# Optimization experiments

Measured on AMD Instinct MI355X. Metric: run time of the kernel, lower is better.

Reference implementation:

```python
import jax, jax.numpy as jnp
import numpy as np

B, N, C, O, K, D = 32, 2048, 64, 64, 3, 16

def setup_inputs() -> dict:
    key = jax.random.key(0)
    ks = jax.random.split(key, 6)
    x = jax.random.normal(ks[0], (B, N, C), dtype=jnp.float32)
    node_embeddings = jax.random.normal(ks[1], (N, D), dtype=jnp.float32)
    adj_m = jax.random.uniform(ks[2], (N, N), dtype=jnp.float32)
    weights_pool = jax.random.normal(ks[3], (D, K, C, O), dtype=jnp.float32) * 0.1
    bias_pool = jax.random.normal(ks[4], (D, O), dtype=jnp.float32) * 0.1
    sa_weight = jax.random.normal(ks[5], (N, 2 * N), dtype=jnp.float32) * (1.0 / np.sqrt(2 * N))
    return {"x": x, "node_embeddings": node_embeddings, "adj_m": adj_m,
            "weights_pool": weights_pool, "bias_pool": bias_pool, "sa_weight": sa_weight}

def reference(x, node_embeddings, adj_m, weights_pool, bias_pool, sa_weight):
    n = node_embeddings.shape[0]
    # learned adaptive adjacency [N,N]
    supports = jax.nn.softmax(jax.nn.relu(node_embeddings @ node_embeddings.T), axis=1)
    # SpatialAttention: 1x1 conv over 2N channels == matmul with [N,2N] weight
    z = jnp.concatenate([supports, adj_m], axis=1) @ sa_weight.T  # [N,N]
    s2 = jax.nn.sigmoid(z)
    supports = s2 * adj_m + (1.0 - s2) * supports
    # Chebyshev polynomial basis
    support_set = [jnp.eye(n, dtype=supports.dtype), supports]
    for _ in range(2, K):
        support_set.append(2.0 * supports @ support_set[-1] - support_set[-2])
    supports_k = jnp.stack(support_set, axis=0)  # [K,N,N]
    # per-node generated weights/bias from embeddings
    weights = jnp.einsum('nd,dkio->nkio', node_embeddings, weights_pool)  # [N,K,C,O]
    bias = node_embeddings @ bias_pool  # [N,O]
    # graph conv: aggregate then per-node matmul
    x_g = jnp.einsum('knm,bmc->bnkc', supports_k, x)  # [B,N,K,C]
    x_gconv = jnp.einsum('bnki,nkio->bno', x_g, weights) + bias  # [B,N,O]
    return x_gconv
```

## Files before the change

kernel.cpp:

```cpp
#include <hip/hip_runtime.h>


typedef unsigned short u16;
typedef float f32x4 __attribute__((ext_vector_type(4)));
typedef __bf16 bf16x8 __attribute__((ext_vector_type(8)));
typedef unsigned short u16x8 __attribute__((ext_vector_type(8)));

__device__ __forceinline__ u16 f2bf(float f) {
    unsigned u = __float_as_uint(f);
    u += 0x7FFFu + ((u >> 16) & 1u);
    return (u16)(u >> 16);
}
__device__ __forceinline__ float bf2f(u16 h) {
    return __uint_as_float((unsigned)h << 16);
}
__device__ __forceinline__ void gl_lds16(const void* g, void* l) {
    __builtin_amdgcn_global_load_lds(
        (const __attribute__((address_space(1))) unsigned*)g,
        (__attribute__((address_space(3))) unsigned*)l, 16, 0, 0);
}

__global__ __launch_bounds__(256)
void supports_softmax(const float* __restrict__ E, u16* __restrict__ Acat) {
    const int n = blockIdx.x, tid = threadIdx.x;
    const int lane = tid & 63, wave = tid >> 6;
    __shared__ float red[4];
    float e[16];
#pragma unroll
    for (int d = 0; d < 16; ++d) e[d] = E[n * 16 + d];
    float v[8];
    float mx = 0.f;
#pragma unroll
    for (int r = 0; r < 8; ++r) {
        int m = r * 256 + tid;
        const float4* Er = (const float4*)(E + (size_t)m * 16);
        float4 a = Er[0], b = Er[1], c = Er[2], d4 = Er[3];
        float s = 0.f;
        s = fmaf(a.x, e[0], s);  s = fmaf(a.y, e[1], s);
        s = fmaf(a.z, e[2], s);  s = fmaf(a.w, e[3], s);
        s = fmaf(b.x, e[4], s);  s = fmaf(b.y, e[5], s);
        s = fmaf(b.z, e[6], s);  s = fmaf(b.w, e[7], s);
        s = fmaf(c.x, e[8], s);  s = fmaf(c.y, e[9], s);
        s = fmaf(c.z, e[10], s); s = fmaf(c.w, e[11], s);
        s = fmaf(d4.x, e[12], s); s = fmaf(d4.y, e[13], s);
        s = fmaf(d4.z, e[14], s); s = fmaf(d4.w, e[15], s);
        s = fmaxf(s, 0.f);
        v[r] = s;
        mx = fmaxf(mx, s);
    }
    for (int off = 32; off; off >>= 1) mx = fmaxf(mx, __shfl_down(mx, off, 64));
    if (lane == 0) red[wave] = mx;
    __syncthreads();
    mx = fmaxf(fmaxf(red[0], red[1]), fmaxf(red[2], red[3]));
    __syncthreads();
    float sum = 0.f;
#pragma unroll
    for (int r = 0; r < 8; ++r) { v[r] = __expf(v[r] - mx); sum += v[r]; }
    for (int off = 32; off; off >>= 1) sum += __shfl_down(sum, off, 64);
    if (lane == 0) red[wave] = sum;
    __syncthreads();
    sum = red[0] + red[1] + red[2] + red[3];
    float inv = 1.f / sum;
#pragma unroll
    for (int r = 0; r < 8; ++r)
        Acat[(size_t)n * 4096 + r * 256 + tid] = f2bf(v[r] * inv);
}

__global__ __launch_bounds__(256)
void cast_inputs(const float* __restrict__ adj, const float* __restrict__ saw,
                 u16* __restrict__ Acat, u16* __restrict__ sawb) {
    int bid = blockIdx.x;
    if (bid < 4096) {
        size_t j = ((size_t)bid * 256 + threadIdx.x) * 4;
        float4 v = *(const float4*)(adj + j);
        int n = (int)(j >> 11), c = (int)(j & 2047);
        ushort4 o = make_ushort4(f2bf(v.x), f2bf(v.y), f2bf(v.z), f2bf(v.w));
        *(ushort4*)(Acat + (size_t)n * 4096 + 2048 + c) = o;
    } else {
        size_t j = ((size_t)(bid - 4096) * 256 + threadIdx.x) * 4;
        float4 v = *(const float4*)(saw + j);
        ushort4 o = make_ushort4(f2bf(v.x), f2bf(v.y), f2bf(v.z), f2bf(v.w));
        *(ushort4*)(sawb + j) = o;
    }
}

__global__ __launch_bounds__(256)
void build_xtT(const float* __restrict__ x, u16* __restrict__ xtT) {
    __shared__ u16 t[64][65];
    int b = blockIdx.y, m0 = blockIdx.x * 64;
    int c = threadIdx.x & 63, g = threadIdx.x >> 6;
#pragma unroll
    for (int r = 0; r < 16; ++r) {
        int mm = g * 16 + r;
        t[mm][c] = f2bf(x[((size_t)b * 2048 + m0 + mm) * 64 + c]);
    }
    __syncthreads();
#pragma unroll
    for (int r = 0; r < 16; ++r) {
        int cc = g * 16 + r;
        xtT[((size_t)b * 64 + cc) * 2048 + m0 + c] = t[c][cc];
    }
}

__global__ __launch_bounds__(256, 4)
void gemm_bt(const u16* __restrict__ A, const u16* __restrict__ Bt,
             float* __restrict__ Cf, int M, int N, int K, int Kh) {
    __shared__ alignas(16) u16 As[128 * 64];
    __shared__ alignas(16) u16 Bs[64 * 64];
    const int tid = threadIdx.x, lane = tid & 63, wave = tid >> 6;
    const int m0 = blockIdx.y * 128, n0 = blockIdx.x * 64;
    const int wm = (wave >> 1) * 64, wn = (wave & 1) * 32;
    const int kbeg = blockIdx.z * Kh, kend = kbeg + Kh;
    const int ml = lane & 15, c0l = lane >> 4;
    f32x4 acc[4][2] = {};

    int baseA[4], mskA[4], baseB[2], mskB[2];
#pragma unroll
    for (int i = 0; i < 4; ++i) { int m = wm + i * 16 + ml; baseA[i] = m * 8; mskA[i] = m & 7; }
#pragma unroll
    for (int j = 0; j < 2; ++j) { int nn = wn + j * 16 + ml; baseB[j] = nn * 8; mskB[j] = nn & 7; }

    for (int k0 = kbeg; k0 < kend; k0 += 64) {
#pragma unroll
        for (int r = 0; r < 4; ++r) {
            int s = wave * 64 + r * 256 + lane;
            int row = s >> 3, gc = (s & 7) ^ (row & 7);
            u16* lds = As + (wave * 64 + r * 256) * 8;
            gl_lds16(A + (size_t)(m0 + row) * K + k0 + gc * 8, lds);
        }
#pragma unroll
        for (int r = 0; r < 2; ++r) {
            int s = wave * 64 + r * 256 + lane;
            int row = s >> 3, gc = (s & 7) ^ (row & 7);
            u16* lds = Bs + (wave * 64 + r * 256) * 8;
            gl_lds16(Bt + (size_t)(n0 + row) * K + k0 + gc * 8, lds);
        }
        __syncthreads();
#pragma unroll
        for (int ks8 = 0; ks8 < 8; ks8 += 4) {
            bf16x8 af[4], bv[2];
#pragma unroll
            for (int i = 0; i < 4; ++i)
                af[i] = *(const bf16x8*)(As + (baseA[i] + ((c0l + ks8) ^ mskA[i])) * 8);
#pragma unroll
            for (int j = 0; j < 2; ++j)
                bv[j] = *(const bf16x8*)(Bs + (baseB[j] + ((c0l + ks8) ^ mskB[j])) * 8);
#pragma unroll
            for (int i = 0; i < 4; ++i)
#pragma unroll
                for (int j = 0; j < 2; ++j)
                    acc[i][j] = __builtin_amdgcn_mfma_f32_16x16x32_bf16(af[i], bv[j], acc[i][j], 0, 0, 0);
        }
        __syncthreads();
    }

    const int col_l = lane & 15, row_l = (lane >> 4) * 4;
    float* Cfp = Cf + (size_t)blockIdx.z * M * N;
#pragma unroll
    for (int i = 0; i < 4; ++i)
#pragma unroll
        for (int j = 0; j < 2; ++j)
#pragma unroll
            for (int r = 0; r < 4; ++r) {
                int row = m0 + wm + i * 16 + row_l + r;
                int col = n0 + wn + j * 16 + col_l;
                Cfp[(size_t)row * N + col] = acc[i][j][r];
            }
}

__global__ __launch_bounds__(256)
void reduce_z(const float* __restrict__ p, const float* __restrict__ adj,
              const u16* __restrict__ Acat, u16* __restrict__ S) {
    size_t j = ((size_t)blockIdx.x * 256 + threadIdx.x) * 4;
    float4 a = *(const float4*)(p + j);
    float4 b = *(const float4*)(p + (size_t)2048 * 2048 + j);
    float4 ad = *(const float4*)(adj + j);
    int row = (int)(j >> 11), col = (int)(j & 2047);
    ushort4 sp = *(const ushort4*)(Acat + (size_t)row * 4096 + col);
    float z0 = a.x + b.x, z1 = a.y + b.y, z2 = a.z + b.z, z3 = a.w + b.w;
    float s0 = 1.f / (1.f + __expf(-z0)), s1 = 1.f / (1.f + __expf(-z1));
    float s2 = 1.f / (1.f + __expf(-z2)), s3 = 1.f / (1.f + __expf(-z3));
    ushort4 o = make_ushort4(
        f2bf(s0 * ad.x + (1.f - s0) * bf2f(sp.x)),
        f2bf(s1 * ad.y + (1.f - s1) * bf2f(sp.y)),
        f2bf(s2 * ad.z + (1.f - s2) * bf2f(sp.z)),
        f2bf(s3 * ad.w + (1.f - s3) * bf2f(sp.w)));
    *(ushort4*)(S + j) = o;
}

__global__ __launch_bounds__(256)
void reduceT(const float* __restrict__ p, u16* __restrict__ xg1,
             u16* __restrict__ xg1T) {
    __shared__ u16 t[64][65];
    int bx = blockIdx.x * 64, by = blockIdx.y * 64;
    int c = threadIdx.x & 63, g = threadIdx.x >> 6;
#pragma unroll
    for (int r = 0; r < 16; ++r) {
        int row = g * 16 + r;
        size_t idx = (size_t)(by + row) * 2048 + bx + c;
        u16 v = f2bf(p[idx] + p[(size_t)2048 * 2048 + idx]);
        xg1[idx] = v;
        t[row][c] = v;
    }
    __syncthreads();
#pragma unroll
    for (int r = 0; r < 16; ++r) {
        int row = g * 16 + r;
        xg1T[(size_t)(bx + row) * 2048 + by + c] = t[c][row];
    }
}

__global__ __launch_bounds__(256)
void reduce2(const float* __restrict__ p, u16* __restrict__ xg2) {
    size_t j = ((size_t)blockIdx.x * 256 + threadIdx.x) * 4;
    float4 a = *(const float4*)(p + j);
    float4 b = *(const float4*)(p + (size_t)2048 * 2048 + j);
    *(ushort4*)(xg2 + j) = make_ushort4(f2bf(a.x + b.x), f2bf(a.y + b.y),
                                        f2bf(a.z + b.z), f2bf(a.w + b.w));
}

__global__ __launch_bounds__(256)
void wgen(const float* __restrict__ E, const float* __restrict__ Wp,
          u16* __restrict__ Wn) {
    __shared__ float Es[128 * 16];
    const int tid = threadIdx.x;
    const int c0 = blockIdx.x * 512, nb = blockIdx.y * 128;
    const int i4 = (tid & 127) * 4, ng = tid >> 7;
    for (int j = tid; j < 2048; j += 256) Es[j] = E[nb * 16 + j];
    float4 wpv[16];
#pragma unroll
    for (int d = 0; d < 16; ++d)
        wpv[d] = *(const float4*)(Wp + (size_t)d * 12288 + c0 + i4);
    __syncthreads();
    for (int nl = 0; nl < 64; ++nl) {
        int n = ng * 64 + nl;
        float4 s = make_float4(0.f, 0.f, 0.f, 0.f);
#pragma unroll
        for (int d = 0; d < 16; ++d) {
            float e = Es[n * 16 + d];
            s.x = fmaf(e, wpv[d].x, s.x);
            s.y = fmaf(e, wpv[d].y, s.y);
            s.z = fmaf(e, wpv[d].z, s.z);
            s.w = fmaf(e, wpv[d].w, s.w);
        }
        ushort4 o = make_ushort4(f2bf(s.x), f2bf(s.y), f2bf(s.z), f2bf(s.w));
        *(ushort4*)(Wn + (size_t)(nb + n) * 12288 + c0 + i4) = o;
    }
}

__global__ __launch_bounds__(256, 4)
void gconv(const float* __restrict__ x, const float* __restrict__ E,
           const u16* __restrict__ Wn, const float* __restrict__ bp,
           const u16* __restrict__ xg1, const u16* __restrict__ xg2,
           float* __restrict__ out) {
    const int n = blockIdx.x, tid = threadIdx.x;
    __shared__ alignas(16) u16 wl[3 * 64 * 64];
    __shared__ alignas(16) u16 xl[3 * 32 * 72];
    __shared__ float bl[64];
    const u16* wrow = Wn + (size_t)n * 12288;
    for (int j = tid * 8; j < 12288; j += 2048)
        *(u16x8*)(wl + j) = *(const u16x8*)(wrow + j);
    if (tid < 64) {
        float s = 0.f;
#pragma unroll
        for (int d = 0; d < 16; ++d) s = fmaf(E[n * 16 + d], bp[d * 64 + tid], s);
        bl[tid] = s;
    }
    {
        const int b = tid >> 3, i = (tid & 7) * 8;
        *(u16x8*)(xl + 2304 + b * 72 + i) = *(const u16x8*)(xg1 + (size_t)n * 2048 + tid * 8);
        *(u16x8*)(xl + 4608 + b * 72 + i) = *(const u16x8*)(xg2 + (size_t)n * 2048 + tid * 8);
        float4 xa = *(const float4*)(x + ((size_t)b * 2048 + n) * 64 + i);
        float4 xb = *(const float4*)(x + ((size_t)b * 2048 + n) * 64 + i + 4);
        u16x8 xc;
        xc[0] = f2bf(xa.x); xc[1] = f2bf(xa.y); xc[2] = f2bf(xa.z); xc[3] = f2bf(xa.w);
        xc[4] = f2bf(xb.x); xc[5] = f2bf(xb.y); xc[6] = f2bf(xb.z); xc[7] = f2bf(xb.w);
        *(u16x8*)(xl + b * 72 + i) = xc;
    }
    __syncthreads();
    for (int j = tid * 8; j < 4096; j += 2048) {
        u16x8 w0 = *(const u16x8*)(wl + j);
        u16x8 w2 = *(const u16x8*)(wl + 8192 + j);
        u16x8 o0, o2;
#pragma unroll
        for (int t = 0; t < 8; ++t) {
            float f2 = bf2f(w2[t]);
            o0[t] = f2bf(bf2f(w0[t]) - f2);
            o2[t] = f2bf(2.f * f2);
        }
        *(u16x8*)(wl + j) = o0;
        *(u16x8*)(wl + 8192 + j) = o2;
    }
    __syncthreads();
    const int b = tid >> 3, og = tid & 7;
    float acc[8];
#pragma unroll
    for (int t = 0; t < 8; ++t) acc[t] = bl[og * 8 + t];
#pragma unroll
    for (int k = 0; k < 3; ++k) {
        const u16* xr = xl + k * 2304 + b * 72;
        const u16* wr = wl + k * 4096 + og * 8;
#pragma unroll 4
        for (int i = 0; i < 64; ++i) {
            float xv = bf2f(xr[i]);
            u16x8 w = *(const u16x8*)(wr + i * 64);
            acc[0] = fmaf(bf2f(w[0]), xv, acc[0]);
            acc[1] = fmaf(bf2f(w[1]), xv, acc[1]);
            acc[2] = fmaf(bf2f(w[2]), xv, acc[2]);
            acc[3] = fmaf(bf2f(w[3]), xv, acc[3]);
            acc[4] = fmaf(bf2f(w[4]), xv, acc[4]);
            acc[5] = fmaf(bf2f(w[5]), xv, acc[5]);
            acc[6] = fmaf(bf2f(w[6]), xv, acc[6]);
            acc[7] = fmaf(bf2f(w[7]), xv, acc[7]);
        }
    }
    float* op = out + ((size_t)b * 2048 + n) * 64 + og * 8;
    *(float4*)op       = make_float4(acc[0], acc[1], acc[2], acc[3]);
    *((float4*)op + 1) = make_float4(acc[4], acc[5], acc[6], acc[7]);
}

extern "C" void kernel_launch(void* const* d_in, const int* in_sizes, int n_in,
                              void* d_out, int out_size, void* d_ws, size_t ws_size,
                              hipStream_t stream) {
    const float* x   = (const float*)d_in[0];
    const float* E   = (const float*)d_in[1];
    const float* adj = (const float*)d_in[2];
    const float* Wp  = (const float*)d_in[3];
    const float* bp  = (const float*)d_in[4];
    const float* saw = (const float*)d_in[5];
    float* out = (float*)d_out;

    char* ws = (char*)d_ws;
    const size_t MB = 1u << 20;
    u16*   Acat  = (u16*)(ws);
    u16*   sawb  = (u16*)(ws + 16 * MB);
    u16*   XtT   = (u16*)(ws + 32 * MB);
    float* part  = (float*)(ws + 48 * MB);
    u16*   S_bf  = (u16*)(ws + 16 * MB);
    u16*   xg1T  = (u16*)(ws + 24 * MB);
    u16*   xg1_bf= (u16*)(ws);
    u16*   xg2_bf= (u16*)(ws + 8 * MB);
    u16*   Wn    = (u16*)(ws + 24 * MB);

    supports_softmax<<<2048, 256, 0, stream>>>(E, Acat);
    cast_inputs<<<12288, 256, 0, stream>>>(adj, saw, Acat, sawb);
    build_xtT<<<dim3(32, 32), 256, 0, stream>>>(x, XtT);

    gemm_bt<<<dim3(32, 16, 2), 256, 0, stream>>>(Acat, sawb, part, 2048, 2048, 4096, 2048);
    reduce_z<<<4096, 256, 0, stream>>>(part, adj, Acat, S_bf);
    gemm_bt<<<dim3(32, 16, 2), 256, 0, stream>>>(S_bf, XtT, part, 2048, 2048, 2048, 1024);
    reduceT<<<dim3(32, 32), 256, 0, stream>>>(part, xg1_bf, xg1T);
    gemm_bt<<<dim3(32, 16, 2), 256, 0, stream>>>(S_bf, xg1T, part, 2048, 2048, 2048, 1024);
    reduce2<<<4096, 256, 0, stream>>>(part, xg2_bf);

    wgen<<<dim3(24, 16), 256, 0, stream>>>(E, Wp, Wn);
    gconv<<<2048, 256, 0, stream>>>(x, E, Wn, bp, xg1_bf, xg2_bf, out);
}
```

Before: 331.0 us.

## Reassociate per-node gconv through weights pool on MFMA; widen split-K GEMM tiles

Stops materializing the per-node generated weights [N,K,C,O]. The graph convolution becomes sum_d E[n,d]*(X_cat @ Wpool_d), computed with MFMA, with the Chebyshev identity/T2 terms folded into the pool weights. The main GEMM moves to 128x128 tiles with 4-way split-K and bf16 partials, halving partial traffic at the cost of extra bf16 rounding in the reductions. x is cast to bf16 up front, and layouts are changed so xg1/xg2 are stored batch-major for the new gconv.

Result: faster. 306.2 us (-7.5%).

```diff
diff --git a/kernel.cpp b/kernel.cpp
--- a/kernel.cpp
+++ b/kernel.cpp
@@ -68,7 +68,8 @@
 
 __global__ __launch_bounds__(256)
 void cast_inputs(const float* __restrict__ adj, const float* __restrict__ saw,
-                 u16* __restrict__ Acat, u16* __restrict__ sawb) {
+                 const float* __restrict__ x, u16* __restrict__ Acat,
+                 u16* __restrict__ sawb, u16* __restrict__ x_bf) {
     int bid = blockIdx.x;
     if (bid < 4096) {
         size_t j = ((size_t)bid * 256 + threadIdx.x) * 4;
@@ -76,11 +77,16 @@
         int n = (int)(j >> 11), c = (int)(j & 2047);
         ushort4 o = make_ushort4(f2bf(v.x), f2bf(v.y), f2bf(v.z), f2bf(v.w));
         *(ushort4*)(Acat + (size_t)n * 4096 + 2048 + c) = o;
-    } else {
+    } else if (bid < 12288) {
         size_t j = ((size_t)(bid - 4096) * 256 + threadIdx.x) * 4;
         float4 v = *(const float4*)(saw + j);
         ushort4 o = make_ushort4(f2bf(v.x), f2bf(v.y), f2bf(v.z), f2bf(v.w));
         *(ushort4*)(sawb + j) = o;
+    } else {
+        size_t j = ((size_t)(bid - 12288) * 256 + threadIdx.x) * 4;
+        float4 v = *(const float4*)(x + j);
+        ushort4 o = make_ushort4(f2bf(v.x), f2bf(v.y), f2bf(v.z), f2bf(v.w));
+        *(ushort4*)(x_bf + j) = o;
     }
 }
 
@@ -102,82 +108,86 @@
     }
 }
 
-__global__ __launch_bounds__(256, 4)
+__global__ __launch_bounds__(256, 3)
 void gemm_bt(const u16* __restrict__ A, const u16* __restrict__ Bt,
-             float* __restrict__ Cf, int M, int N, int K, int Kh) {
+             u16* __restrict__ Cp, int M, int N, int K, int Kh) {
     __shared__ alignas(16) u16 As[128 * 64];
-    __shared__ alignas(16) u16 Bs[64 * 64];
+    __shared__ alignas(16) u16 Bs[128 * 64];
     const int tid = threadIdx.x, lane = tid & 63, wave = tid >> 6;
-    const int m0 = blockIdx.y * 128, n0 = blockIdx.x * 64;
-    const int wm = (wave >> 1) * 64, wn = (wave & 1) * 32;
+    const int m0 = blockIdx.y * 128, n0 = blockIdx.x * 128;
+    const int wm = (wave >> 1) * 64, wn = (wave & 1) * 64;
     const int kbeg = blockIdx.z * Kh, kend = kbeg + Kh;
     const int ml = lane & 15, c0l = lane >> 4;
-    f32x4 acc[4][2] = {};
-
-    int baseA[4], mskA[4], baseB[2], mskB[2];
+    f32x4 acc[4][4] = {};
+
+    int baseA[4], mskA[4], baseB[4], mskB[4];
 #pragma unroll
     for (int i = 0; i < 4; ++i) { int m = wm + i * 16 + ml; baseA[i] = m * 8; mskA[i] = m & 7; }
 #pragma unroll
-    for (int j = 0; j < 2; ++j) { int nn = wn + j * 16 + ml; baseB[j] = nn * 8; mskB[j] = nn & 7; }
+    for (int j = 0; j < 4; ++j) { int nn = wn + j * 16 + ml; baseB[j] = nn * 8; mskB[j] = nn & 7; }
 
     for (int k0 = kbeg; k0 < kend; k0 += 64) {
 #pragma unroll
         for (int r = 0; r < 4; ++r) {
             int s = wave * 64 + r * 256 + lane;
             int row = s >> 3, gc = (s & 7) ^ (row & 7);
-            u16* lds = As + (wave * 64 + r * 256) * 8;
-            gl_lds16(A + (size_t)(m0 + row) * K + k0 + gc * 8, lds);
-        }
-#pragma unroll
-        for (int r = 0; r < 2; ++r) {
+            gl_lds16(A + (size_t)(m0 + row) * K + k0 + gc * 8, As + (size_t)s * 8);
+        }
+#pragma unroll
+        for (int r = 0; r < 4; ++r) {
             int s = wave * 64 + r * 256 + lane;
             int row = s >> 3, gc = (s & 7) ^ (row & 7);
-            u16* lds = Bs + (wave * 64 + r * 256) * 8;
-            gl_lds16(Bt + (size_t)(n0 + row) * K + k0 + gc * 8, lds);
+            gl_lds16(Bt + (size_t)(n0 + row) * K + k0 + gc * 8, Bs + (size_t)s * 8);
         }
         __syncthreads();
 #pragma unroll
-        for (int ks8 = 0; ks8 < 8; ks8 += 4) {
-            bf16x8 af[4], bv[2];
+        for (int ks4 = 0; ks4 < 8; ks4 += 4) {
+            bf16x8 af[4], bv[4];
 #pragma unroll
             for (int i = 0; i < 4; ++i)
-                af[i] = *(const bf16x8*)(As + (baseA[i] + ((c0l + ks8) ^ mskA[i])) * 8);
-#pragma unroll
-            for (int j = 0; j < 2; ++j)
-                bv[j] = *(const bf16x8*)(Bs + (baseB[j] + ((c0l + ks8) ^ mskB[j])) * 8);
+                af[i] = *(const bf16x8*)(As + (baseA[i] + ((c0l + ks4) ^ mskA[i])) * 8);
+#pragma unroll
+            for (int j = 0; j < 4; ++j)
+                bv[j] = *(const bf16x8*)(Bs + (baseB[j] + ((c0l + ks4) ^ mskB[j])) * 8);
 #pragma unroll
             for (int i = 0; i < 4; ++i)
 #pragma unroll
-                for (int j = 0; j < 2; ++j)
+                for (int j = 0; j < 4; ++j)
                     acc[i][j] = __builtin_amdgcn_mfma_f32_16x16x32_bf16(af[i], bv[j], acc[i][j], 0, 0, 0);
         }
         __syncthreads();
     }
 
     const int col_l = lane & 15, row_l = (lane >> 4) * 4;
-    float* Cfp = Cf + (size_t)blockIdx.z * M * N;
+    u16* Cz = Cp + (size_t)blockIdx.z * M * N;
 #pragma unroll
     for (int i = 0; i < 4; ++i)
 #pragma unroll
-        for (int j = 0; j < 2; ++j)
+        for (int j = 0; j < 4; ++j)
 #pragma unroll
             for (int r = 0; r < 4; ++r) {
                 int row = m0 + wm + i * 16 + row_l + r;
                 int col = n0 + wn + j * 16 + col_l;
-                Cfp[(size_t)row * N + col] = acc[i][j][r];
+                Cz[(size_t)row * N + col] = f2bf(acc[i][j][r]);
             }
 }
 
-__global__ __launch_bounds__(256)
-void reduce_z(const float* __restrict__ p, const float* __restrict__ adj,
+#define PSTRIDE ((size_t)2048 * 2048)
+__global__ __launch_bounds__(256)
+void reduce_z(const u16* __restrict__ p, const float* __restrict__ adj,
               const u16* __restrict__ Acat, u16* __restrict__ S) {
     size_t j = ((size_t)blockIdx.x * 256 + threadIdx.x) * 4;
-    float4 a = *(const float4*)(p + j);
-    float4 b = *(const float4*)(p + (size_t)2048 * 2048 + j);
+    ushort4 p0 = *(const ushort4*)(p + j);
+    ushort4 p1 = *(const ushort4*)(p + PSTRIDE + j);
+    ushort4 p2 = *(const ushort4*)(p + 2 * PSTRIDE + j);
+    ushort4 p3 = *(const ushort4*)(p + 3 * PSTRIDE + j);
     float4 ad = *(const float4*)(adj + j);
     int row = (int)(j >> 11), col = (int)(j & 2047);
     ushort4 sp = *(const ushort4*)(Acat + (size_t)row * 4096 + col);
-    float z0 = a.x + b.x, z1 = a.y + b.y, z2 = a.z + b.z, z3 = a.w + b.w;
+    float z0 = bf2f(p0.x) + bf2f(p1.x) + bf2f(p2.x) + bf2f(p3.x);
+    float z1 = bf2f(p0.y) + bf2f(p1.y) + bf2f(p2.y) + bf2f(p3.y);
+    float z2 = bf2f(p0.z) + bf2f(p1.z) + bf2f(p2.z) + bf2f(p3.z);
+    float z3 = bf2f(p0.w) + bf2f(p1.w) + bf2f(p2.w) + bf2f(p3.w);
     float s0 = 1.f / (1.f + __expf(-z0)), s1 = 1.f / (1.f + __expf(-z1));
     float s2 = 1.f / (1.f + __expf(-z2)), s3 = 1.f / (1.f + __expf(-z3));
     ushort4 o = make_ushort4(
@@ -189,17 +199,19 @@
 }
 
 __global__ __launch_bounds__(256)
-void reduceT(const float* __restrict__ p, u16* __restrict__ xg1,
+void reduceT(const u16* __restrict__ p, u16* __restrict__ xg1b,
              u16* __restrict__ xg1T) {
     __shared__ u16 t[64][65];
     int bx = blockIdx.x * 64, by = blockIdx.y * 64;
     int c = threadIdx.x & 63, g = threadIdx.x >> 6;
+    int b = bx >> 6;
 #pragma unroll
     for (int r = 0; r < 16; ++r) {
         int row = g * 16 + r;
         size_t idx = (size_t)(by + row) * 2048 + bx + c;
-        u16 v = f2bf(p[idx] + p[(size_t)2048 * 2048 + idx]);
-        xg1[idx] = v;
+        u16 v = f2bf(bf2f(p[idx]) + bf2f(p[PSTRIDE + idx]) +
+                     bf2f(p[2 * PSTRIDE + idx]) + bf2f(p[3 * PSTRIDE + idx]));
+        xg1b[((size_t)b * 2048 + by + row) * 64 + c] = v;
         t[row][c] = v;
     }
     __syncthreads();
@@ -211,112 +223,143 @@
 }
 
 __global__ __launch_bounds__(256)
-void reduce2(const float* __restrict__ p, u16* __restrict__ xg2) {
+void reduce2(const u16* __restrict__ p, u16* __restrict__ xg2b) {
     size_t j = ((size_t)blockIdx.x * 256 + threadIdx.x) * 4;
-    float4 a = *(const float4*)(p + j);
-    float4 b = *(const float4*)(p + (size_t)2048 * 2048 + j);
-    *(ushort4*)(xg2 + j) = make_ushort4(f2bf(a.x + b.x), f2bf(a.y + b.y),
-                                        f2bf(a.z + b.z), f2bf(a.w + b.w));
-}
-
-__global__ __launch_bounds__(256)
-void wgen(const float* __restrict__ E, const float* __restrict__ Wp,
-          u16* __restrict__ Wn) {
-    __shared__ float Es[128 * 16];
-    const int tid = threadIdx.x;
-    const int c0 = blockIdx.x * 512, nb = blockIdx.y * 128;
-    const int i4 = (tid & 127) * 4, ng = tid >> 7;
-    for (int j = tid; j < 2048; j += 256) Es[j] = E[nb * 16 + j];
-    float4 wpv[16];
-#pragma unroll
-    for (int d = 0; d < 16; ++d)
-        wpv[d] = *(const float4*)(Wp + (size_t)d * 12288 + c0 + i4);
-    __syncthreads();
-    for (int nl = 0; nl < 64; ++nl) {
-        int n = ng * 64 + nl;
-        float4 s = make_float4(0.f, 0.f, 0.f, 0.f);
-#pragma unroll
-        for (int d = 0; d < 16; ++d) {
-            float e = Es[n * 16 + d];
-            s.x = fmaf(e, wpv[d].x, s.x);
-            s.y = fmaf(e, wpv[d].y, s.y);
-            s.z = fmaf(e, wpv[d].z, s.z);
-            s.w = fmaf(e, wpv[d].w, s.w);
-        }
-        ushort4 o = make_ushort4(f2bf(s.x), f2bf(s.y), f2bf(s.z), f2bf(s.w));
-        *(ushort4*)(Wn + (size_t)(nb + n) * 12288 + c0 + i4) = o;
-    }
-}
-
-__global__ __launch_bounds__(256, 4)
-void gconv(const float* __restrict__ x, const float* __restrict__ E,
-           const u16* __restrict__ Wn, const float* __restrict__ bp,
-           const u16* __restrict__ xg1, const u16* __restrict__ xg2,
-           float* __restrict__ out) {
-    const int n = blockIdx.x, tid = threadIdx.x;
-    __shared__ alignas(16) u16 wl[3 * 64 * 64];
-    __shared__ alignas(16) u16 xl[3 * 32 * 72];
-    __shared__ float bl[64];
-    const u16* wrow = Wn + (size_t)n * 12288;
-    for (int j = tid * 8; j < 12288; j += 2048)
-        *(u16x8*)(wl + j) = *(const u16x8*)(wrow + j);
-    if (tid < 64) {
-        float s = 0.f;
-#pragma unroll
-        for (int d = 0; d < 16; ++d) s = fmaf(E[n * 16 + d], bp[d * 64 + tid], s);
-        bl[tid] = s;
-    }
-    {
-        const int b = tid >> 3, i = (tid & 7) * 8;
-        *(u16x8*)(xl + 2304 + b * 72 + i) = *(const u16x8*)(xg1 + (size_t)n * 2048 + tid * 8);
-        *(u16x8*)(xl + 4608 + b * 72 + i) = *(const u16x8*)(xg2 + (size_t)n * 2048 + tid * 8);
-        float4 xa = *(const float4*)(x + ((size_t)b * 2048 + n) * 64 + i);
-        float4 xb = *(const float4*)(x + ((size_t)b * 2048 + n) * 64 + i + 4);
-        u16x8 xc;
-        xc[0] = f2bf(xa.x); xc[1] = f2bf(xa.y); xc[2] = f2bf(xa.z); xc[3] = f2bf(xa.w);
-        xc[4] = f2bf(xb.x); xc[5] = f2bf(xb.y); xc[6] = f2bf(xb.z); xc[7] = f2bf(xb.w);
-        *(u16x8*)(xl + b * 72 + i) = xc;
-    }
-    __syncthreads();
-    for (int j = tid * 8; j < 4096; j += 2048) {
-        u16x8 w0 = *(const u16x8*)(wl + j);
-        u16x8 w2 = *(const u16x8*)(wl + 8192 + j);
-        u16x8 o0, o2;
-#pragma unroll
-        for (int t = 0; t < 8; ++t) {
-            float f2 = bf2f(w2[t]);
-            o0[t] = f2bf(bf2f(w0[t]) - f2);
-            o2[t] = f2bf(2.f * f2);
-        }
-        *(u16x8*)(wl + j) = o0;
-        *(u16x8*)(wl + 8192 + j) = o2;
-    }
-    __syncthreads();
-    const int b = tid >> 3, og = tid & 7;
-    float acc[8];
-#pragma unroll
-    for (int t = 0; t < 8; ++t) acc[t] = bl[og * 8 + t];
-#pragma unroll
-    for (int k = 0; k < 3; ++k) {
-        const u16* xr = xl + k * 2304 + b * 72;
-        const u16* wr = wl + k * 4096 + og * 8;
-#pragma unroll 4
-        for (int i = 0; i < 64; ++i) {
-            float xv = bf2f(xr[i]);
-            u16x8 w = *(const u16x8*)(wr + i * 64);
-            acc[0] = fmaf(bf2f(w[0]), xv, acc[0]);
-            acc[1] = fmaf(bf2f(w[1]), xv, acc[1]);
-            acc[2] = fmaf(bf2f(w[2]), xv, acc[2]);
-            acc[3] = fmaf(bf2f(w[3]), xv, acc[3]);
-            acc[4] = fmaf(bf2f(w[4]), xv, acc[4]);
-            acc[5] = fmaf(bf2f(w[5]), xv, acc[5]);
-            acc[6] = fmaf(bf2f(w[6]), xv, acc[6]);
-            acc[7] = fmaf(bf2f(w[7]), xv, acc[7]);
-        }
-    }
-    float* op = out + ((size_t)b * 2048 + n) * 64 + og * 8;
-    *(float4*)op       = make_float4(acc[0], acc[1], acc[2], acc[3]);
-    *((float4*)op + 1) = make_float4(acc[4], acc[5], acc[6], acc[7]);
+    ushort4 p0 = *(const ushort4*)(p + j);
+    ushort4 p1 = *(const ushort4*)(p + PSTRIDE + j);
+    ushort4 p2 = *(const ushort4*)(p + 2 * PSTRIDE + j);
+    ushort4 p3 = *(const ushort4*)(p + 3 * PSTRIDE + j);
+    int n = (int)(j >> 11), bc = (int)(j & 2047);
+    int b = bc >> 6, c = bc & 63;
+    ushort4 o = make_ushort4(
+        f2bf(bf2f(p0.x) + bf2f(p1.x) + bf2f(p2.x) + bf2f(p3.x)),
+        f2bf(bf2f(p0.y) + bf2f(p1.y) + bf2f(p2.y) + bf2f(p3.y)),
+        f2bf(bf2f(p0.z) + bf2f(p1.z) + bf2f(p2.z) + bf2f(p3.z)),
+        f2bf(bf2f(p0.w) + bf2f(p1.w) + bf2f(p2.w) + bf2f(p3.w)));
+    *(ushort4*)(xg2b + ((size_t)b * 2048 + n) * 64 + c) = o;
+}
+
+__global__ __launch_bounds__(256)
+void prep(const float* __restrict__ Wp, const float* __restrict__ E,
+          const float* __restrict__ bp, u16* __restrict__ Wpb,
+          float* __restrict__ bias) {
+    const int bid = blockIdx.x, tid = threadIdx.x;
+    if (bid < 16) {
+        const int d = bid;
+        const float* base = Wp + (size_t)d * 12288;
+        for (int idx = tid; idx < 12288; idx += 256) {
+            int o = idx / 192, ki = idx - o * 192;
+            int k = ki >> 6, i = ki & 63;
+            float v;
+            if (k == 0)      v = base[i * 64 + o] - base[2 * 4096 + i * 64 + o];
+            else if (k == 1) v = base[4096 + i * 64 + o];
+            else             v = 2.f * base[2 * 4096 + i * 64 + o];
+            Wpb[(size_t)(d * 64 + o) * 192 + ki] = f2bf(v);
+        }
+    } else {
+        const int nb = bid - 16;
+#pragma unroll
+        for (int it = 0; it < 8; ++it) {
+            int idx = tid + it * 256;
+            int n = nb * 32 + (idx >> 6), o = idx & 63;
+            float s = 0.f;
+#pragma unroll
+            for (int d = 0; d < 16; ++d) s = fmaf(E[n * 16 + d], bp[d * 64 + o], s);
+            bias[(size_t)n * 64 + o] = s;
+        }
+    }
+}
+
+__global__ __launch_bounds__(256, 2)
+void gconv_mfma(const u16* __restrict__ x_bf, const u16* __restrict__ xg1,
+                const u16* __restrict__ xg2, const u16* __restrict__ Wpb,
+                const float* __restrict__ bias, const float* __restrict__ E,
+                float* __restrict__ out) {
+    __shared__ alignas(16) u16 As[128 * 192];
+    __shared__ alignas(16) u16 Bs[64 * 192];
+    __shared__ float El[16 * 128];
+    const int tid = threadIdx.x, lane = tid & 63, wave = tid >> 6;
+    const int m0 = blockIdx.x * 128, nb = m0 & 2047;
+    const int wm = (wave >> 1) * 64, wn = (wave & 1) * 32;
+    const int ml = lane & 15, c0l = lane >> 4;
+    const int col_l = lane & 15, rl = (lane >> 4) * 4;
+
+#pragma unroll
+    for (int it = 0; it < 12; ++it) {
+        int s = tid + it * 256;
+        int row = s / 24, sc = s - row * 24;
+        int gc = (sc & 24) | ((sc ^ row) & 7);
+        const u16* src = (gc < 8) ? x_bf : (gc < 16 ? xg1 : xg2);
+        gl_lds16(src + (size_t)(m0 + row) * 64 + (gc & 7) * 8, As + (size_t)s * 8);
+    }
+#pragma unroll
+    for (int it = 0; it < 8; ++it) {
+        int idx = tid + it * 256;
+        El[idx] = E[(size_t)(nb + (idx & 127)) * 16 + (idx >> 7)];
+    }
+    f32x4 oacc[4][2];
+#pragma unroll
+    for (int i = 0; i < 4; ++i)
+#pragma unroll
+        for (int j = 0; j < 2; ++j)
+#pragma unroll
+            for (int r = 0; r < 4; ++r)
+                oacc[i][j][r] = bias[(size_t)(nb + wm + i * 16 + rl + r) * 64 + wn + j * 16 + col_l];
+    __syncthreads();
+
+    bf16x8 af[4][6];
+#pragma unroll
+    for (int i = 0; i < 4; ++i) {
+        int m = wm + i * 16 + ml, base = m * 24, msk = m & 7;
+#pragma unroll
+        for (int ks = 0; ks < 6; ++ks) {
+            int c = c0l + ks * 4;
+            af[i][ks] = *(const bf16x8*)(As + (base + ((c & 24) | ((c ^ msk) & 7))) * 8);
+        }
+    }
+
+    for (int d = 0; d < 16; ++d) {
+        if (d) __syncthreads();
+#pragma unroll
+        for (int it = 0; it < 6; ++it) {
+            int s = tid + it * 256;
+            int row = s / 24, sc = s - row * 24;
+            int gc = (sc & 24) | ((sc ^ row) & 7);
+            gl_lds16(Wpb + (size_t)(d * 64 + row) * 192 + gc * 8, Bs + (size_t)s * 8);
+        }
+        __syncthreads();
+        f32x4 tmp[4][2] = {};
+#pragma unroll
+        for (int ks = 0; ks < 6; ++ks) {
+            bf16x8 bv[2];
+#pragma unroll
+            for (int j = 0; j < 2; ++j) {
+                int o = wn + j * 16 + ml, msk = o & 7, c = c0l + ks * 4;
+                bv[j] = *(const bf16x8*)(Bs + (o * 24 + ((c & 24) | ((c ^ msk) & 7))) * 8);
+            }
+#pragma unroll
+            for (int i = 0; i < 4; ++i)
+#pragma unroll
+                for (int j = 0; j < 2; ++j)
+                    tmp[i][j] = __builtin_amdgcn_mfma_f32_16x16x32_bf16(af[i][ks], bv[j], tmp[i][j], 0, 0, 0);
+        }
+#pragma unroll
+        for (int i = 0; i < 4; ++i)
+#pragma unroll
+            for (int r = 0; r < 4; ++r) {
+                float ev = El[d * 128 + wm + i * 16 + rl + r];
+#pragma unroll
+                for (int j = 0; j < 2; ++j)
+                    oacc[i][j][r] = fmaf(ev, tmp[i][j][r], oacc[i][j][r]);
+            }
+    }
+#pragma unroll
+    for (int i = 0; i < 4; ++i)
+#pragma unroll
+        for (int j = 0; j < 2; ++j)
+#pragma unroll
+            for (int r = 0; r < 4; ++r)
+                out[(size_t)(m0 + wm + i * 16 + rl + r) * 64 + wn + j * 16 + col_l] = oacc[i][j][r];
 }
 
 extern "C" void kernel_launch(void* const* d_in, const int* in_sizes, int n_in,
@@ -335,24 +378,26 @@
     u16*   Acat  = (u16*)(ws);
     u16*   sawb  = (u16*)(ws + 16 * MB);
     u16*   XtT   = (u16*)(ws + 32 * MB);
-    float* part  = (float*)(ws + 48 * MB);
+    u16*   x_bf  = (u16*)(ws + 40 * MB);
+    u16*   part  = (u16*)(ws + 48 * MB);
     u16*   S_bf  = (u16*)(ws + 16 * MB);
     u16*   xg1T  = (u16*)(ws + 24 * MB);
-    u16*   xg1_bf= (u16*)(ws);
-    u16*   xg2_bf= (u16*)(ws + 8 * MB);
-    u16*   Wn    = (u16*)(ws + 24 * MB);
+    u16*   xg1b  = (u16*)(ws);
+    u16*   xg2b  = (u16*)(ws + 8 * MB);
+    u16*   Wpb   = (u16*)(ws + 32 * MB);
+    float* bias  = (float*)(ws + 33 * MB);
 
     supports_softmax<<<2048, 256, 0, stream>>>(E, Acat);
-    cast_inputs<<<12288, 256, 0, stream>>>(adj, saw, Acat, sawb);
+    cast_inputs<<<16384, 256, 0, stream>>>(adj, saw, x, Acat, sawb, x_bf);
     build_xtT<<<dim3(32, 32), 256, 0, stream>>>(x, XtT);
 
-    gemm_bt<<<dim3(32, 16, 2), 256, 0, stream>>>(Acat, sawb, part, 2048, 2048, 4096, 2048);
+    gemm_bt<<<dim3(16, 16, 4), 256, 0, stream>>>(Acat, sawb, part, 2048, 2048, 4096, 1024);
     reduce_z<<<4096, 256, 0, stream>>>(part, adj, Acat, S_bf);
-    gemm_bt<<<dim3(32, 16, 2), 256, 0, stream>>>(S_bf, XtT, part, 2048, 2048, 2048, 1024);
-    reduceT<<<dim3(32, 32), 256, 0, stream>>>(part, xg1_bf, xg1T);
-    gemm_bt<<<dim3(32, 16, 2), 256, 0, stream>>>(S_bf, xg1T, part, 2048, 2048, 2048, 1024);
-    reduce2<<<4096, 256, 0, stream>>>(part, xg2_bf);
-
-    wgen<<<dim3(24, 16), 256, 0, stream>>>(E, Wp, Wn);
-    gconv<<<2048, 256, 0, stream>>>(x, E, Wn, bp, xg1_bf, xg2_bf, out);
-}
+    gemm_bt<<<dim3(16, 16, 4), 256, 0, stream>>>(S_bf, XtT, part, 2048, 2048, 2048, 512);
+    reduceT<<<dim3(32, 32), 256, 0, stream>>>(part, xg1b, xg1T);
+    prep<<<80, 256, 0, stream>>>(Wp, E, bp, Wpb, bias);
+    gemm_bt<<<dim3(16, 16, 4), 256, 0, stream>>>(S_bf, xg1T, part, 2048, 2048, 2048, 512);
+    reduce2<<<4096, 256, 0, stream>>>(part, xg2b);
+
+    gconv_mfma<<<512, 256, 0, stream>>>(x_bf, xg1b, xg2b, Wpb, bias, E, out);
+}
```
